# Kernel tuning notes

Measured on AMD Instinct MI355X. Metric: run time of the kernel, lower is better.

The kernel has to match this reference:

```python
import jax, jax.numpy as jnp
import numpy as np

N = 100000   # num_nodes
D = 128      # input_dim
DO = 128     # output_dim
V = 3        # num_views/relations
E = 500000   # edges per view
C = 2        # num_classes
H = D // 2   # label-attention hidden
VH = DO // 2 # view-attention hidden
EPS = 1e-5


def setup_inputs() -> dict:
    key = jax.random.key(0)
    ks = jax.random.split(key, 20)
    s = 0.05
    def nrm(k, shape):
        return jax.random.normal(k, shape, dtype=jnp.float32) * s
    return {
        'features': jax.random.normal(ks[0], (N, D), dtype=jnp.float32),
        'edge_src': jax.random.randint(ks[1], (V, E), 0, N, dtype=jnp.int32),
        'edge_dst': jax.random.randint(ks[2], (V, E), 0, N, dtype=jnp.int32),
        'edge_w': jax.random.uniform(ks[3], (V, E), dtype=jnp.float32),
        'clsW': nrm(ks[4], (D, C)), 'clsb': jnp.zeros((C,), jnp.float32),
        'attW1': nrm(ks[5], (C, D, H)), 'attb1': jnp.zeros((C, H), jnp.float32),
        'attW2': nrm(ks[6], (C, H)), 'attb2': jnp.zeros((C,), jnp.float32),
        'att_bias': jnp.float32(0.1),
        'relW': nrm(ks[7], (V, D, DO)), 'relb': jnp.zeros((V, DO), jnp.float32),
        'gateW': nrm(ks[8], (V, DO, DO)), 'gateb': jnp.zeros((V, DO), jnp.float32),
        'view_pref': jax.random.normal(ks[9], (V, DO), dtype=jnp.float32),
        'vattW1': nrm(ks[10], (DO, VH)), 'vattb1': jnp.zeros((VH,), jnp.float32),
        'vattW2': nrm(ks[11], (VH,)), 'vattb2': jnp.float32(0.0),
        'selfW': nrm(ks[12], (D, DO)), 'selfb': jnp.zeros((DO,), jnp.float32),
        'featW': nrm(ks[13], (D, DO)), 'featb': jnp.zeros((DO,), jnp.float32),
        'fusW': nrm(ks[14], (2 * DO, DO)), 'fusb': jnp.zeros((DO,), jnp.float32),
        'ln_g': jnp.ones((DO,), jnp.float32), 'ln_b': jnp.zeros((DO,), jnp.float32),
    }


def reference(features, edge_src, edge_dst, edge_w,
              clsW, clsb, attW1, attb1, attW2, attb2, att_bias,
              relW, relb, gateW, gateb,
              view_pref, vattW1, vattb1, vattW2, vattb2,
              selfW, selfb, featW, featb, fusW, fusb, ln_g, ln_b):
    # --- LabelAwareAttention ---
    class_probs = jax.nn.softmax(features @ clsW + clsb, axis=-1)          # [N,C]
    h = jax.nn.relu(jnp.einsum('nd,cdh->cnh', features, attW1) + attb1[:, None, :])
    scores = jax.nn.sigmoid(jnp.einsum('cnh,ch->cn', h, attW2) + attb2[:, None])
    node_att = jnp.sum(scores.T * class_probs, axis=-1) + att_bias         # [N]

    # --- per-view RelationAggregator (num_relations=1 -> relation weight is 1) ---
    src_f = features[edge_src]                                             # [V,E,D]
    msg = (jnp.einsum('ved,vdo->veo', src_f, relW) + relb[:, None, :]) \
          * edge_w[..., None]                                              # [V,E,DO]
    agg = jax.vmap(lambda m, d: jax.ops.segment_sum(m, d, num_segments=N))(
        msg, edge_dst)                                                     # [V,N,DO]
    gate = jax.nn.sigmoid(jnp.einsum('vno,vop->vnp', agg, gateW) + gateb[:, None, :])
    view_out = gate * agg                                                  # [V,N,DO]

    # --- ViewLevelAttention ---
    vh = jax.nn.relu(jnp.einsum('vno,oh->vnh', view_out * view_pref[:, None, :], vattW1) + vattb1)
    vscores = jnp.einsum('vnh,h->vn', vh, vattW2) + vattb2                 # [V,N]
    vweights = jax.nn.softmax(vscores, axis=0)                             # softmax over views
    combined = jnp.sum(view_out * vweights[..., None], axis=0)             # [N,DO]

    # --- fusion + residual + layer norm (dropout=0, eval) ---
    self_out = features @ selfW + selfb
    transformed = features @ featW + featb
    weighted = combined * node_att[:, None]
    fused = jax.nn.relu(jnp.concatenate([self_out, weighted], axis=-1) @ fusW + fusb)
    out = fused + transformed
    mu = jnp.mean(out, axis=-1, keepdims=True)
    var = jnp.var(out, axis=-1, keepdims=True)
    out = (out - mu) / jnp.sqrt(var + EPS) * ln_g + ln_b
    return out, class_probs
```

## Files before the change

kernel.cpp:

```cpp
#include <hip/hip_runtime.h>
#include <hip/hip_bf16.h>

#define NN 100000
#define DD 128
#define VV 3
#define EE 500000
#define TOT (VV * NN)
#define NB ((TOT + 255) / 256)
#define RGB ((NN + 127) / 128)

typedef unsigned short u16;
typedef unsigned int u32;
typedef short s8v __attribute__((ext_vector_type(8)));
typedef float f4v __attribute__((ext_vector_type(4)));

__device__ __forceinline__ float bf2f(u16 u) {
    return __uint_as_float(((u32)u) << 16);
}
__device__ __forceinline__ u16 f2bf(float f) {
    u32 x = __float_as_uint(f);
    u32 r = (x + 0x7fffu + ((x >> 16) & 1u)) >> 16;
    return (u16)r;
}

// ... 64 lines not shown
        int flat = rep * NT + tid;
        int kk = flat >> 5;
        int c4 = flat & 31;
        float4 q = *reinterpret_cast<const float4*>(src + kk * 128 + c4 * 4);
        *reinterpret_cast<float4*>(Ws + kk * WSTR + c4 * 4) = q;
    }
}

template<int XSTR, int NT>
__device__ __forceinline__ void stage_x_f32(float* Xs, const float* __restrict__ src, int tid) {
    #pragma unroll
    for (int rep = 0; rep < 1024 / NT; ++rep) {
        int flat = rep * NT + tid;
        int n = flat >> 5;
        int c4 = flat & 31;
        float4 q = *reinterpret_cast<const float4*>(src + (size_t)n * 128 + c4 * 4);
        *reinterpret_cast<float4*>(Xs + n * XSTR + c4 * 4) = q;
    }
}

template<int XSTR, int NT>
__device__ __forceinline__ void stage_x_bf16(float* Xs, const u16* __restrict__ src, int tid) {
    #pragma unroll
    for (int rep = 0; rep < 512 / NT; ++rep) {
        int flat = rep * NT + tid;
        int n = flat >> 4;
        int c8 = flat & 15;
        uint4 q = *reinterpret_cast<const uint4*>(src + (size_t)n * 128 + c8 * 8);
        float* d = Xs + n * XSTR + c8 * 8;
        d[0] = bf2f((u16)(q.x & 0xffffu)); d[1] = bf2f((u16)(q.x >> 16));
        d[2] = bf2f((u16)(q.y & 0xffffu)); d[3] = bf2f((u16)(q.y >> 16));
        d[4] = bf2f((u16)(q.z & 0xffffu)); d[5] = bf2f((u16)(q.z >> 16));
        d[6] = bf2f((u16)(q.w & 0xffffu)); d[7] = bf2f((u16)(q.w >> 16));
    }
}

__global__ void prep_kernel(const float* __restrict__ selfW, const float* __restrict__ selfb,
                            const float* __restrict__ fusW, const float* __restrict__ fusb,
                            float* __restrict__ Wsf, float* __restrict__ c1) {
    int o = threadIdx.x;
    int k = blockIdx.x;
    if (k < 128) {
        float acc = 0.f;
        for (int m = 0; m < 128; ++m)
            acc += selfW[k * 128 + m] * fusW[m * 128 + o];
        Wsf[k * 128 + o] = acc;
    } else {
        float acc = 0.f;
        for (int m = 0; m < 128; ++m)
            acc += selfb[m] * fusW[m * 128 + o];
        c1[o] = acc + fusb[o];
    }
}

__global__ __launch_bounds__(128) void wprep_kernel(
        const float* __restrict__ relW, const float* __restrict__ gateW,
        u16* __restrict__ relWb, u16* __restrict__ gateWb) {
    int k = threadIdx.x;
    int n = blockIdx.x & 127;
    int v = blockIdx.x >> 7;
    size_t o = ((size_t)v * 128 + n) * 128 + k;
    size_t i = ((size_t)v * 128 + k) * 128 + n;
    relWb[o]  = f2bf(relW[i]);
    gateWb[o] = f2bf(gateW[i]);
}

// ... 180 lines not shown
        u16* __restrict__ aggB, float* __restrict__ wsum) {
    long long t = (long long)blockIdx.x * 256 + threadIdx.x;
    int lane = (int)(t & 31);
    int eg = (int)(t >> 5);
    int v = eg / EE;
    int src = 0, dst = 0; float w = 0.f;
    if (lane == 0) {
        src = esrc[eg]; dst = edst[eg]; w = ew[eg];
    }
    src = __shfl(src, 0, 32);
    dst = __shfl(dst, 0, 32);
    w   = __shfl(w, 0, 32);
    const float* fr = feat + (size_t)src * DD + lane * 4;
    float4 q = *reinterpret_cast<const float4*>(fr);
    u16* outp = aggB + ((size_t)v * NN + dst) * DD + lane * 4;
    atomAddBf16x2(outp,     w * q.x, w * q.y);
    atomAddBf16x2(outp + 2, w * q.z, w * q.w);
    if (lane == 0) atomicAdd(wsum + v * NN + dst, w);
}

__global__ __launch_bounds__(256) void label_mfma_kernel(
        const u16* __restrict__ featB, const u16* __restrict__ attW1B,
        const float* __restrict__ clsW, const float* __restrict__ clsb,
        const float* __restrict__ attb1, const float* __restrict__ attW2,
        const float* __restrict__ attb2, const float* __restrict__ att_bias,
        float* __restrict__ node_att, float* __restrict__ probs_out) {
    __shared__ u16 Xs[128][136];
    __shared__ u16 Wt[128][72];
    int tid = threadIdx.x;
    int wv = tid >> 6, lane = tid & 63;
    int quad = lane >> 4, l15 = lane & 15;
    int row0 = blockIdx.x * 128;

    #pragma unroll
    for (int rep = 0; rep < 8; ++rep) {
        int flat = rep * 256 + tid;
        int n = flat >> 4, c8 = flat & 15;
        int gr = row0 + n; if (gr >= NN) gr = NN - 1;
        uint4 q = *reinterpret_cast<const uint4*>(featB + (size_t)gr * DD + c8 * 8);
        *reinterpret_cast<uint4*>(&Xs[n][c8 * 8]) = q;
    }

    f4v acc[2][8];
    #pragma unroll
    for (int rt = 0; rt < 2; ++rt)
        #pragma unroll
        for (int c = 0; c < 8; ++c)
            acc[rt][c] = f4v{0.f, 0.f, 0.f, 0.f};

    #pragma unroll
    for (int h = 0; h < 2; ++h) {
        #pragma unroll
        for (int rep = 0; rep < 4; ++rep) {
            int flat = rep * 256 + tid;
            int n = flat >> 3, c8 = flat & 7;
            uint4 q = *reinterpret_cast<const uint4*>(attW1B + (size_t)n * DD + h * 64 + c8 * 8);
            *reinterpret_cast<uint4*>(&Wt[n][c8 * 8]) = q;
        }
        __syncthreads();
        #pragma unroll
        for (int t = 0; t < 2; ++t) {
            int kl = t * 32 + quad * 8;
            s8v a0 = *reinterpret_cast<const s8v*>(&Xs[wv * 32 + l15][h * 64 + kl]);
            s8v a1 = *reinterpret_cast<const s8v*>(&Xs[wv * 32 + 16 + l15][h * 64 + kl]);
            #pragma unroll
            for (int c = 0; c < 8; ++c) {
                s8v b = *reinterpret_cast<const s8v*>(&Wt[c * 16 + l15][kl]);
                acc[0][c] = __builtin_amdgcn_mfma_f32_16x16x32_bf16(a0, b, acc[0][c], 0, 0, 0);
                acc[1][c] = __builtin_amdgcn_mfma_f32_16x16x32_bf16(a1, b, acc[1][c], 0, 0, 0);
            }
        }
        __syncthreads();
    }

    float ab1[8], aw2[8];
    #pragma unroll
    for (int c = 0; c < 8; ++c) {
        int col = c * 16 + l15;
        ab1[c] = attb1[col];
        aw2[c] = attW2[col];
    }
    float cw0[8], cw1[8];
    #pragma unroll
    for (int j = 0; j < 8; ++j) {
        int k = l15 * 8 + j;
        cw0[j] = clsW[k * 2];
        cw1[j] = clsW[k * 2 + 1];
    }
    float cb0 = clsb[0], cb1 = clsb[1];
    float b20 = attb2[0], b21 = attb2[1];
    float abias = att_bias[0];

    #pragma unroll
    for (int rt = 0; rt < 2; ++rt)
        #pragma unroll
        for (int r = 0; r < 4; ++r) {
            int n = wv * 32 + rt * 16 + quad * 4 + r;
            int gr = row0 + n;
            float p0 = 0.f, p1 = 0.f;
            #pragma unroll
            for (int c = 0; c < 4; ++c) {
                float hv = acc[rt][c][r] + ab1[c];
                hv = hv > 0.f ? hv : 0.f;
                p0 += hv * aw2[c];
            }
            #pragma unroll
// ... 93 lines not shown
    __syncthreads();
    if (tid < 64) {
        int n = tid >> 1, cc = tid & 1;
        float l = 0.f;
        for (int k = 0; k < 128; k += 4) {
            float4 x = *reinterpret_cast<const float4*>(&Xs[n][k]);
            l += x.x * clsW[(k + 0) * 2 + cc];
            l += x.y * clsW[(k + 1) * 2 + cc];
            l += x.z * clsW[(k + 2) * 2 + cc];
            l += x.w * clsW[(k + 3) * 2 + cc];
        }
        Lsc[n * 2 + cc] = l + clsb[cc];
        float s = 0.f;
        for (int u = 0; u < 16; ++u) s += red[n * 33 + cc * 16 + u];
        s += attb2[cc];
        Ssc[n * 2 + cc] = 1.f / (1.f + expf(-s));
    }
    __syncthreads();
    if (tid < 32) {
        int n = tid;
        float l0 = Lsc[n * 2], l1 = Lsc[n * 2 + 1];
        float m = fmaxf(l0, l1);
        float e0 = expf(l0 - m), e1 = expf(l1 - m);
        float inv = 1.f / (e0 + e1);
        float p0 = e0 * inv, p1 = e1 * inv;
        float na = p0 * Ssc[n * 2] + p1 * Ssc[n * 2 + 1] + att_bias[0];
        int row = row0 + n;
        node_att[row] = na;
        probs_out[row * 2]     = p0;
        probs_out[row * 2 + 1] = p1;
    }
}

__global__ __launch_bounds__(256, 3) void relgate_mfma_kernel(
        const u16* __restrict__ relWb, const float* __restrict__ relb,
        const u16* __restrict__ W12b, const float* __restrict__ rgb,
        const float* __restrict__ gateb,
        const u16* __restrict__ vattW1p, const float* __restrict__ vattb1,
        const float* __restrict__ vattW2, const float* __restrict__ vattb2,
        u16* __restrict__ aggB, const float* __restrict__ wsum,
        float* __restrict__ vscores) {
    __shared__ u16 Wf[128][136];
    __shared__ u16 Wt[128][72];
    int tid = threadIdx.x;
    int wv = tid >> 6, lane = tid & 63;
    int quad = lane >> 4, l15 = lane & 15;
    int v = blockIdx.y;
    int row0 = blockIdx.x * 128;
    const size_t vbase = (size_t)v * NN;

    #pragma unroll
    for (int rep = 0; rep < 8; ++rep) {
        int flat = rep * 256 + tid;
        int n = flat >> 4, c8 = flat & 15;
        int gr = row0 + n; if (gr >= NN) gr = NN - 1;
        uint4 q = *reinterpret_cast<const uint4*>(aggB + (vbase + gr) * DD + c8 * 8);
        *reinterpret_cast<uint4*>(&Wf[n][c8 * 8]) = q;
    }
    __syncthreads();

    s8v af[2][2][2];
    #pragma unroll
    for (int h = 0; h < 2; ++h)
        #pragma unroll
        for (int t = 0; t < 2; ++t) {
            int kl = h * 64 + t * 32 + quad * 8;
            af[h][t][0] = *reinterpret_cast<const s8v*>(&Wf[wv * 32 + l15][kl]);
            af[h][t][1] = *reinterpret_cast<const s8v*>(&Wf[wv * 32 + 16 + l15][kl]);
        }
    __syncthreads();

    const u16* W1 = relWb + (size_t)v * DD * DD;
    const u16* W2 = W12b + (size_t)v * DD * DD;
    #pragma unroll
    for (int rep = 0; rep < 8; ++rep) {
        int flat = rep * 256 + tid;
        int n = flat >> 4, c8 = flat & 15;
        *reinterpret_cast<uint4*>(&Wf[n][c8 * 8]) =
            *reinterpret_cast<const uint4*>(W1 + (size_t)n * DD + c8 * 8);
    }
    #pragma unroll
    for (int rep = 0; rep < 4; ++rep) {
        int flat = rep * 256 + tid;
        int n = flat >> 3, c8 = flat & 7;
        *reinterpret_cast<uint4*>(&Wt[n][c8 * 8]) =
            *reinterpret_cast<const uint4*>(W2 + (size_t)n * DD + c8 * 8);
    }
    __syncthreads();

    f4v acc1[2][8], acc2[2][8];
    #pragma unroll
    for (int rt = 0; rt < 2; ++rt)
        #pragma unroll
        for (int c = 0; c < 8; ++c) {
            acc1[rt][c] = f4v{0.f, 0.f, 0.f, 0.f};
            acc2[rt][c] = f4v{0.f, 0.f, 0.f, 0.f};
        }

    #pragma unroll
    for (int h = 0; h < 2; ++h)
        #pragma unroll
        for (int t = 0; t < 2; ++t) {
            int kl = h * 64 + t * 32 + quad * 8;
            #pragma unroll
            for (int c = 0; c < 8; ++c) {
                s8v b = *reinterpret_cast<const s8v*>(&Wf[c * 16 + l15][kl]);
                acc1[0][c] = __builtin_amdgcn_mfma_f32_16x16x32_bf16(af[h][t][0], b, acc1[0][c], 0, 0, 0);
                acc1[1][c] = __builtin_amdgcn_mfma_f32_16x16x32_bf16(af[h][t][1], b, acc1[1][c], 0, 0, 0);
            }
        }
    #pragma unroll
    for (int t = 0; t < 2; ++t) {
        int kl = t * 32 + quad * 8;
        #pragma unroll
        for (int c = 0; c < 8; ++c) {
            s8v b = *reinterpret_cast<const s8v*>(&Wt[c * 16 + l15][kl]);
            acc2[0][c] = __builtin_amdgcn_mfma_f32_16x16x32_bf16(af[0][t][0], b, acc2[0][c], 0, 0, 0);
            acc2[1][c] = __builtin_amdgcn_mfma_f32_16x16x32_bf16(af[0][t][1], b, acc2[1][c], 0, 0, 0);
        }
    }
    __syncthreads();

    #pragma unroll
    for (int rep = 0; rep < 4; ++rep) {
        int flat = rep * 256 + tid;
        int n = flat >> 3, c8 = flat & 7;
        *reinterpret_cast<uint4*>(&Wt[n][c8 * 8]) =
            *reinterpret_cast<const uint4*>(W2 + (size_t)n * DD + 64 + c8 * 8);
    }
    __syncthreads();
    #pragma unroll
    for (int t = 0; t < 2; ++t) {
        int kl = t * 32 + quad * 8;
        #pragma unroll
        for (int c = 0; c < 8; ++c) {
            s8v b = *reinterpret_cast<const s8v*>(&Wt[c * 16 + l15][kl]);
            acc2[0][c] = __builtin_amdgcn_mfma_f32_16x16x32_bf16(af[1][t][0], b, acc2[0][c], 0, 0, 0);
            acc2[1][c] = __builtin_amdgcn_mfma_f32_16x16x32_bf16(af[1][t][1], b, acc2[1][c], 0, 0, 0);
        }
    }

    float wsn[2][4];
    #pragma unroll
    for (int rt = 0; rt < 2; ++rt)
        #pragma unroll
        for (int r = 0; r < 4; ++r) {
            int gr = row0 + wv * 32 + rt * 16 + quad * 4 + r;
            wsn[rt][r] = wsum[vbase + (gr < NN ? gr : NN - 1)];
        }
    float rb[8], rg2[8], gb[8];
    #pragma unroll
    for (int c = 0; c < 8; ++c) {
        int col = c * 16 + l15;
        rb[c]  = relb[v * DD + col];
        rg2[c] = rgb[v * DD + col];
        gb[c]  = gateb[v * DD + col];
    }
    #pragma unroll
    for (int rt = 0; rt < 2; ++rt)
        #pragma unroll
        for (int c = 0; c < 8; ++c)
            #pragma unroll
            for (int r = 0; r < 4; ++r) {
                float a = acc1[rt][c][r] + wsn[rt][r] * rb[c];
                float g = fsigmoid(acc2[rt][c][r] + wsn[rt][r] * rg2[c] + gb[c]);
                Wf[wv * 32 + rt * 16 + quad * 4 + r][c * 16 + l15] = f2bf(g * a);
            }
    __syncthreads();

    {
        const u16* Wv = vattW1p + (size_t)v * 64 * DD;
        #pragma unroll
        for (int rep = 0; rep < 4; ++rep) {
            int flat = rep * 256 + tid;
            int n = flat >> 4, c8 = flat & 15;
            uint4 q = *reinterpret_cast<const uint4*>(Wv + (size_t)n * DD + c8 * 8);
            int half = c8 >> 3;
            *reinterpret_cast<uint4*>(&Wt[half * 64 + n][(c8 & 7) * 8]) = q;
        }
    }
    s8v a2[2][2][2];
    #pragma unroll
    for (int h = 0; h < 2; ++h)
        #pragma unroll
        for (int t = 0; t < 2; ++t) {
            int kl = h * 64 + t * 32 + quad * 8;
            a2[h][t][0] = *reinterpret_cast<const s8v*>(&Wf[wv * 32 + l15][kl]);
            a2[h][t][1] = *reinterpret_cast<const s8v*>(&Wf[wv * 32 + 16 + l15][kl]);
        }
    #pragma unroll
    for (int rep = 0; rep < 8; ++rep) {
        int flat = rep * 256 + tid;
        int n = flat >> 4, c8 = flat & 15;
        int gr = row0 + n;
        if (gr < NN)
            *reinterpret_cast<uint4*>(aggB + (vbase + gr) * DD + c8 * 8) =
                *reinterpret_cast<const uint4*>(&Wf[n][c8 * 8]);
    }
    __syncthreads();

    f4v acc3[2][4];
    #pragma unroll
    for (int rt = 0; rt < 2; ++rt)
        #pragma unroll
        for (int c = 0; c < 4; ++c)
            acc3[rt][c] = f4v{0.f, 0.f, 0.f, 0.f};
    #pragma unroll
    for (int h = 0; h < 2; ++h)
        #pragma unroll
        for (int t = 0; t < 2; ++t) {
            int kl = t * 32 + quad * 8;
            #pragma unroll
            for (int c = 0; c < 4; ++c) {
                s8v b = *reinterpret_cast<const s8v*>(&Wt[h * 64 + c * 16 + l15][kl]);
                acc3[0][c] = __builtin_amdgcn_mfma_f32_16x16x32_bf16(a2[h][t][0], b, acc3[0][c], 0, 0, 0);
                acc3[1][c] = __builtin_amdgcn_mfma_f32_16x16x32_bf16(a2[h][t][1], b, acc3[1][c], 0, 0, 0);
            }
        }
    float vb1[4], vw2[4];
    #pragma unroll
    for (int c = 0; c < 4; ++c) {
        int col = c * 16 + l15;
        vb1[c] = vattb1[col];
        vw2[c] = vattW2[col];
    }
    float vb2 = vattb2[0];
    #pragma unroll
    for (int rt = 0; rt < 2; ++rt)
        #pragma unroll
        for (int r = 0; r < 4; ++r) {
            float p = 0.f;
            #pragma unroll
            for (int c = 0; c < 4; ++c) {
                float hv = acc3[rt][c][r] + vb1[c];
                hv = hv > 0.f ? hv : 0.f;
                p += hv * vw2[c];
            }
            #pragma unroll
            for (int m = 1; m < 16; m <<= 1)
                p += __shfl_xor(p, m);
            int gr = row0 + wv * 32 + rt * 16 + quad * 4 + r;
            if (l15 == 0 && gr < NN)
                vscores[vbase + gr] = p + vb2;
        }
}

__global__ __launch_bounds__(256) void relgate_kernel(
        const float* __restrict__ relW, const float* __restrict__ relb,
        const float* __restrict__ gateW, const float* __restrict__ gateb,
        u16* __restrict__ aggB, const float* __restrict__ wsum) {
    __shared__ float Xs[32][128];
    __shared__ float Ws[64][132];
    int tid = threadIdx.x;
    int v = blockIdx.y;
    int row0 = blockIdx.x * 32;
    u16* base = aggB + ((size_t)v * NN + row0) * DD;
    stage_x_bf16<128, 256>(&Xs[0][0], base, tid);
    int to = tid & 31, tn = tid >> 5;
    int o0 = to * 4, n0 = tn * 4;
    float acc[4][4] = {};
    const float* W1 = relW + (size_t)v * DD * DD;
    for (int half = 0; half < 2; ++half) {
        __syncthreads();
        stage_w_f32<132, 256>(&Ws[0][0], W1 + half * 64 * DD, tid);
        __syncthreads();
        gemm16<128, 132>(acc, &Xs[0][0], &Ws[0][0], n0, o0, half * 64);
    }
    float wsn[4], rb[4];
    #pragma unroll
    for (int i = 0; i < 4; ++i) wsn[i] = wsum[v * NN + row0 + n0 + i];
    #pragma unroll
    for (int j = 0; j < 4; ++j) rb[j] = relb[v * DD + o0 + j];
    #pragma unroll
    for (int i = 0; i < 4; ++i)
        #pragma unroll
        for (int j = 0; j < 4; ++j) acc[i][j] += wsn[i] * rb[j];
    __syncthreads();
// ... 159 lines not shown
        #pragma unroll
        for (int t = 0; t < 2; ++t) {
            int kl = h * 64 + t * 32 + quad * 8;
            af[h][t][0] = *reinterpret_cast<const s8v*>(&Wf[wv * 32 + l15][kl]);
            af[h][t][1] = *reinterpret_cast<const s8v*>(&Wf[wv * 32 + 16 + l15][kl]);
        }
    __syncthreads();

    #pragma unroll
    for (int rep = 0; rep < 8; ++rep) {
        int flat = rep * 256 + tid;
        int n = flat >> 4, c8 = flat & 15;
        *reinterpret_cast<uint4*>(&Wf[n][c8 * 8]) =
            *reinterpret_cast<const uint4*>(WsfB + (size_t)n * DD + c8 * 8);
    }
    #pragma unroll
    for (int rep = 0; rep < 4; ++rep) {
        int flat = rep * 256 + tid;
        int n = flat >> 3, c8 = flat & 7;
        *reinterpret_cast<uint4*>(&Wt[n][c8 * 8]) =
            *reinterpret_cast<const uint4*>(featWB + (size_t)n * DD + c8 * 8);
    }
    __syncthreads();

    f4v acc1[2][8], acc2[2][8];
    #pragma unroll
    for (int rt = 0; rt < 2; ++rt)
        #pragma unroll
        for (int c = 0; c < 8; ++c) {
            acc1[rt][c] = f4v{0.f, 0.f, 0.f, 0.f};
            acc2[rt][c] = f4v{0.f, 0.f, 0.f, 0.f};
        }

    #pragma unroll
    for (int h = 0; h < 2; ++h)
        #pragma unroll
        for (int t = 0; t < 2; ++t) {
            int kl = h * 64 + t * 32 + quad * 8;
            #pragma unroll
            for (int c = 0; c < 8; ++c) {
                s8v b = *reinterpret_cast<const s8v*>(&Wf[c * 16 + l15][kl]);
                acc1[0][c] = __builtin_amdgcn_mfma_f32_16x16x32_bf16(af[h][t][0], b, acc1[0][c], 0, 0, 0);
                acc1[1][c] = __builtin_amdgcn_mfma_f32_16x16x32_bf16(af[h][t][1], b, acc1[1][c], 0, 0, 0);
            }
        }
    #pragma unroll
    for (int t = 0; t < 2; ++t) {
        int kl = t * 32 + quad * 8;
        #pragma unroll
        for (int c = 0; c < 8; ++c) {
            s8v b = *reinterpret_cast<const s8v*>(&Wt[c * 16 + l15][kl]);
            acc2[0][c] = __builtin_amdgcn_mfma_f32_16x16x32_bf16(af[0][t][0], b, acc2[0][c], 0, 0, 0);
            acc2[1][c] = __builtin_amdgcn_mfma_f32_16x16x32_bf16(af[0][t][1], b, acc2[1][c], 0, 0, 0);
        }
    }
    __syncthreads();
    #pragma unroll
    for (int rep = 0; rep < 4; ++rep) {
        int flat = rep * 256 + tid;
        int n = flat >> 3, c8 = flat & 7;
        *reinterpret_cast<uint4*>(&Wt[n][c8 * 8]) =
            *reinterpret_cast<const uint4*>(featWB + (size_t)n * DD + 64 + c8 * 8);
    }
    __syncthreads();
    #pragma unroll
    for (int t = 0; t < 2; ++t) {
        int kl = t * 32 + quad * 8;
        #pragma unroll
        for (int c = 0; c < 8; ++c) {
            s8v b = *reinterpret_cast<const s8v*>(&Wt[c * 16 + l15][kl]);
            acc2[0][c] = __builtin_amdgcn_mfma_f32_16x16x32_bf16(af[1][t][0], b, acc2[0][c], 0, 0, 0);
            acc2[1][c] = __builtin_amdgcn_mfma_f32_16x16x32_bf16(af[1][t][1], b, acc2[1][c], 0, 0, 0);
        }
    }

    #pragma unroll
    for (int rep = 0; rep < 8; ++rep) {
        int flat = rep * 256 + tid;
        int n = flat >> 4, c8 = flat & 15;
        int gr = row0 + n; if (gr >= NN) gr = NN - 1;
        size_t off = (size_t)gr * DD + c8 * 8;
        uint4 q0 = *reinterpret_cast<const uint4*>(aggB + off);
        uint4 q1 = *reinterpret_cast<const uint4*>(aggB + (size_t)NN * DD + off);
        uint4 q2 = *reinterpret_cast<const uint4*>(aggB + 2 * (size_t)NN * DD + off);
        const float* rwp = reinterpret_cast<const float*>(&Wf[n][128]);
        float w0 = rwp[0], w1 = rwp[1], w2 = rwp[2];
        u32 o[4];
        const u32* a = &q0.x; const u32* b = &q1.x; const u32* c = &q2.x;
        #pragma unroll
        for (int j = 0; j < 4; ++j) {
            float lo = bf2f((u16)(a[j] & 0xffffu)) * w0 + bf2f((u16)(b[j] & 0xffffu)) * w1
                     + bf2f((u16)(c[j] & 0xffffu)) * w2;
            float hi = bf2f((u16)(a[j] >> 16)) * w0 + bf2f((u16)(b[j] >> 16)) * w1
                     + bf2f((u16)(c[j] >> 16)) * w2;
            o[j] = (u32)f2bf(lo) | ((u32)f2bf(hi) << 16);
        }
        uint4 r; r.x = o[0]; r.y = o[1]; r.z = o[2]; r.w = o[3];
        *reinterpret_cast<uint4*>(&Wf[n][c8 * 8]) = r;
    }
    __syncthreads();

    #pragma unroll
    for (int rep = 0; rep < 4; ++rep) {
        int flat = rep * 256 + tid;
        int n = flat >> 3, c8 = flat & 7;
        *reinterpret_cast<uint4*>(&Wt[n][c8 * 8]) =
            *reinterpret_cast<const uint4*>(fusWbB + (size_t)n * DD + c8 * 8);
// ... 210 lines not shown
    u16* WsfB   = gateWb + (size_t)VV * DD * DD;
    u16* featWB = WsfB + DD * DD;
    u16* fusWbB = featWB + DD * DD;
    u16* attW1B = fusWbB + DD * DD;
    u16* vattW1p = attW1B + DD * DD;
    u16* W12b   = vattW1p + (size_t)VV * 64 * DD;
    float* rgb  = (float*)(W12b + (size_t)VV * DD * DD);
    int*   C    = (int*)(rgb + VV * DD);
    int*   bs   = C + (size_t)TOT;
    int2*  bsw  = (int2*)(bs + NB + 1);
    u16* featB  = (u16*)(bsw + (size_t)VV * EE);
    size_t needed = (size_t)((char*)(featB + (size_t)NN * DD) - (char*)d_ws);

    float* outp  = (float*)d_out;
    float* probs = outp + (size_t)NN * DD;

    prep_kernel<<<129, 128, 0, stream>>>(selfW, selfb, fusW, fusb, Wsf, c1);
    if (ws_size >= needed) {
        featconv_kernel<<<12500, 256, 0, stream>>>(feat, featB);
        wprep_kernel<<<384, 128, 0, stream>>>(relW, gateW, relWb, gateWb);
        wprep2_kernel<<<128, 128, 0, stream>>>(Wsf, featW, fusW, WsfB, featWB, fusWbB);
        wprep3_kernel<<<128, 128, 0, stream>>>(attW1, attW1B);
        wprep4_kernel<<<192, 128, 0, stream>>>(vattW1, view_pref, vattW1p);
        wprep5_kernel<<<VV * 129, 128, 0, stream>>>(relW, gateW, relb, W12b, rgb);
        label_mfma_kernel<<<RGB, 256, 0, stream>>>(featB, attW1B, clsW, clsb, attb1,
                                                   attW2, attb2, att_bias, natt, probs);
        hipMemsetAsync(C, 0, (size_t)TOT * sizeof(int), stream);
        count_kernel<<<(VV * EE + 255) / 256, 256, 0, stream>>>(edst, C);
        scanA_kernel<<<NB, 256, 0, stream>>>(C, bs);
        scanB_kernel<<<1, 1024, 0, stream>>>(bs);
        scanC_kernel<<<NB, 256, 0, stream>>>(C, bs);
        fill_kernel<<<(VV * EE + 255) / 256, 256, 0, stream>>>(esrc, edst, ew, C, bsw);
        gather_kernel<<<(VV * NN) / 4, 256, 0, stream>>>(featB, C, bsw, aggB, wsum);
        relgate_mfma_kernel<<<dim3(RGB, 3), 256, 0, stream>>>(relWb, relb, W12b, rgb, gateb,
                                                              vattW1p, vattb1, vattW2, vattb2,
                                                              aggB, wsum, vsc);
        final_mfma_kernel<<<RGB, 256, 0, stream>>>(featB, aggB, vsc, natt,
                                                   WsfB, featWB, fusWbB,
                                                   c1, featb, ln_g, ln_b, outp);
    } else {
        label_kernel<<<3125, 256, 0, stream>>>(feat, clsW, clsb, attW1, attb1, attW2, attb2,
                                               att_bias, natt, probs);
        hipMemsetAsync(d_ws, 0,
                       (size_t)VV * NN * DD * sizeof(u16) + (size_t)VV * NN * sizeof(float),
                       stream);
        scatter_kernel<<<187500, 256, 0, stream>>>(esrc, edst, ew, feat, aggB, wsum);
        relgate_kernel<<<dim3(3125, 3), 256, 0, stream>>>(relW, relb, gateW, gateb, aggB, wsum);
        vatt_kernel<<<dim3(3125, 3), 128, 0, stream>>>(aggB, view_pref, vattW1, vattb1,
                                                       vattW2, vattb2, vsc);
        combine_kernel<<<12500, 256, 0, stream>>>(aggB, vsc, natt);
        final_kernel<<<3125, 256, 0, stream>>>(feat, aggB, Wsf, c1, fusW, featW, featb,
                                               ln_g, ln_b, outp);
    }
}
```

Measured before the change: 661.3 us.

## Loop views inside relgate kernel, shrink shared memory, load A fragments from global

The relgate MFMA kernel now handles all three views in one block with an in-kernel loop instead of a 3-wide grid. It drops the separate Wt buffer by staging the rel and gate weight halves side by side in one shared tile. A fragments now load straight from global memory, vatt weights are read from global, and launch bounds are raised to 4 blocks per CU to gain occupancy. In exchange the grid shrinks to about 782 blocks, the views run serially inside each block, and extra barriers plus uncoalesced fragment loads are added. Label and final kernels are refactored onto shared helper functions, and label now stages the first weight half together with X under one barrier.

```diff
diff --git a/kernel.cpp b/kernel.cpp
--- a/kernel.cpp
+++ b/kernel.cpp
@@ -120,6 +120,128 @@
         d[2] = bf2f((u16)(q.y & 0xffffu)); d[3] = bf2f((u16)(q.y >> 16));
         d[4] = bf2f((u16)(q.z & 0xffffu)); d[5] = bf2f((u16)(q.z >> 16));
         d[6] = bf2f((u16)(q.w & 0xffffu)); d[7] = bf2f((u16)(q.w >> 16));
+    }
+}
+
+
+__device__ __forceinline__ void stageWf(u16 (*Wf)[136], const u16* __restrict__ src, int tid) {
+    #pragma unroll
+    for (int rep = 0; rep < 8; ++rep) {
+        int flat = rep * 256 + tid;
+        int n = flat >> 4, c8 = flat & 15;
+        *reinterpret_cast<uint4*>(&Wf[n][c8 * 8]) =
+            *reinterpret_cast<const uint4*>(src + (size_t)n * DD + c8 * 8);
+    }
+}
+
+__device__ __forceinline__ void stageWtHalf(u16 (*Wt)[72], const u16* __restrict__ src, int tid) {
+    #pragma unroll
+    for (int rep = 0; rep < 4; ++rep) {
+        int flat = rep * 256 + tid;
+        int n = flat >> 3, c8 = flat & 7;
+        *reinterpret_cast<uint4*>(&Wt[n][c8 * 8]) =
+            *reinterpret_cast<const uint4*>(src + (size_t)n * DD + c8 * 8);
+    }
+}
+
+__device__ __forceinline__ void stageHalf2(u16 (*Wf)[136], const u16* __restrict__ A,
+                                           const u16* __restrict__ B, int tid) {
+    #pragma unroll
+    for (int rep = 0; rep < 4; ++rep) {
+        int flat = rep * 256 + tid;
+        int n = flat >> 3, c8 = flat & 7;
+        *reinterpret_cast<uint4*>(&Wf[n][c8 * 8]) =
+            *reinterpret_cast<const uint4*>(A + (size_t)n * DD + c8 * 8);
+        *reinterpret_cast<uint4*>(&Wf[n][64 + c8 * 8]) =
+            *reinterpret_cast<const uint4*>(B + (size_t)n * DD + c8 * 8);
+    }
+}
+
+__device__ __forceinline__ void stageX(u16 (*Wf)[136], const u16* __restrict__ src,
+                                       int row0, int tid) {
+    #pragma unroll
+    for (int rep = 0; rep < 8; ++rep) {
+        int flat = rep * 256 + tid;
+        int n = flat >> 4, c8 = flat & 15;
+        int gr = row0 + n; if (gr >= NN) gr = NN - 1;
+        *reinterpret_cast<uint4*>(&Wf[n][c8 * 8]) =
+            *reinterpret_cast<const uint4*>(src + (size_t)gr * DD + c8 * 8);
+    }
+}
+
+__device__ __forceinline__ void loadFrags(s8v af[2][2][2], u16 (*Wf)[136],
+                                          int wv, int l15, int quad) {
+    #pragma unroll
+    for (int h = 0; h < 2; ++h)
+        #pragma unroll
+        for (int t = 0; t < 2; ++t) {
+            int kl = h * 64 + t * 32 + quad * 8;
+            af[h][t][0] = *reinterpret_cast<const s8v*>(&Wf[wv * 32 + l15][kl]);
+            af[h][t][1] = *reinterpret_cast<const s8v*>(&Wf[wv * 32 + 16 + l15][kl]);
+        }
+}
+
+__device__ __forceinline__ void loadFragsG(s8v af[2][2][2], const u16* __restrict__ X,
+                                           int row0, int wv, int l15, int quad) {
+    int r0 = row0 + wv * 32 + l15;
+    int r1 = r0 + 16;
+    if (r0 >= NN) r0 = NN - 1;
+    if (r1 >= NN) r1 = NN - 1;
+    #pragma unroll
+    for (int h = 0; h < 2; ++h)
+        #pragma unroll
+        for (int t = 0; t < 2; ++t) {
+            int kl = h * 64 + t * 32 + quad * 8;
+            af[h][t][0] = *reinterpret_cast<const s8v*>(X + (size_t)r0 * DD + kl);
+            af[h][t][1] = *reinterpret_cast<const s8v*>(X + (size_t)r1 * DD + kl);
+        }
+}
+
+__device__ __forceinline__ void mfmaWt8(f4v acc[2][8], const s8v af[2][2][2], int h,
+                                        u16 (*Wt)[72], int l15, int quad) {
+    #pragma unroll
+    for (int t = 0; t < 2; ++t) {
+        int kl = t * 32 + quad * 8;
+        #pragma unroll
+        for (int c = 0; c < 8; ++c) {
+            s8v b = *reinterpret_cast<const s8v*>(&Wt[c * 16 + l15][kl]);
+            acc[0][c] = __builtin_amdgcn_mfma_f32_16x16x32_bf16(af[h][t][0], b, acc[0][c], 0, 0, 0);
+            acc[1][c] = __builtin_amdgcn_mfma_f32_16x16x32_bf16(af[h][t][1], b, acc[1][c], 0, 0, 0);
+        }
+    }
+}
+
+__device__ __forceinline__ void mfmaWfFull(f4v acc[2][8], const s8v af[2][2][2],
+                                           u16 (*Wf)[136], int l15, int quad) {
+    #pragma unroll
+    for (int h = 0; h < 2; ++h)
+        #pragma unroll
+        for (int t = 0; t < 2; ++t) {
+            int kl = h * 64 + t * 32 + quad * 8;
+            #pragma unroll
+            for (int c = 0; c < 8; ++c) {
+                s8v b = *reinterpret_cast<const s8v*>(&Wf[c * 16 + l15][kl]);
+                acc[0][c] = __builtin_amdgcn_mfma_f32_16x16x32_bf16(af[h][t][0], b, acc[0][c], 0, 0, 0);
+                acc[1][c] = __builtin_amdgcn_mfma_f32_16x16x32_bf16(af[h][t][1], b, acc[1][c], 0, 0, 0);
+            }
+        }
+}
+
+__device__ __forceinline__ void mfmaHalf2(f4v acc1[2][8], f4v acc2[2][8],
+                                          const s8v af[2][2][2], int h,
+                                          u16 (*Wf)[136], int l15, int quad) {
+    #pragma unroll
+    for (int t = 0; t < 2; ++t) {
+        int kl = t * 32 + quad * 8;
+        #pragma unroll
+        for (int c = 0; c < 8; ++c) {
+            s8v bA = *reinterpret_cast<const s8v*>(&Wf[c * 16 + l15][kl]);
+            s8v bB = *reinterpret_cast<const s8v*>(&Wf[c * 16 + l15][64 + kl]);
+            acc1[0][c] = __builtin_amdgcn_mfma_f32_16x16x32_bf16(af[h][t][0], bA, acc1[0][c], 0, 0, 0);
+            acc1[1][c] = __builtin_amdgcn_mfma_f32_16x16x32_bf16(af[h][t][1], bA, acc1[1][c], 0, 0, 0);
+            acc2[0][c] = __builtin_amdgcn_mfma_f32_16x16x32_bf16(af[h][t][0], bB, acc2[0][c], 0, 0, 0);
+            acc2[1][c] = __builtin_amdgcn_mfma_f32_16x16x32_bf16(af[h][t][1], bB, acc2[1][c], 0, 0, 0);
+        }
     }
 }
 
@@ -366,46 +488,22 @@
     int quad = lane >> 4, l15 = lane & 15;
     int row0 = blockIdx.x * 128;
 
-    #pragma unroll
-    for (int rep = 0; rep < 8; ++rep) {
-        int flat = rep * 256 + tid;
-        int n = flat >> 4, c8 = flat & 15;
-        int gr = row0 + n; if (gr >= NN) gr = NN - 1;
-        uint4 q = *reinterpret_cast<const uint4*>(featB + (size_t)gr * DD + c8 * 8);
-        *reinterpret_cast<uint4*>(&Xs[n][c8 * 8]) = q;
-    }
-
+    stageX(Xs, featB, row0, tid);
+    stageWtHalf(Wt, attW1B, tid);
+    __syncthreads();
+    s8v af[2][2][2];
+    loadFrags(af, Xs, wv, l15, quad);
     f4v acc[2][8];
     #pragma unroll
     for (int rt = 0; rt < 2; ++rt)
         #pragma unroll
         for (int c = 0; c < 8; ++c)
             acc[rt][c] = f4v{0.f, 0.f, 0.f, 0.f};
-
-    #pragma unroll
-    for (int h = 0; h < 2; ++h) {
-        #pragma unroll
-        for (int rep = 0; rep < 4; ++rep) {
-            int flat = rep * 256 + tid;
-            int n = flat >> 3, c8 = flat & 7;
-            uint4 q = *reinterpret_cast<const uint4*>(attW1B + (size_t)n * DD + h * 64 + c8 * 8);
-            *reinterpret_cast<uint4*>(&Wt[n][c8 * 8]) = q;
-        }
-        __syncthreads();
-        #pragma unroll
-        for (int t = 0; t < 2; ++t) {
-            int kl = t * 32 + quad * 8;
-            s8v a0 = *reinterpret_cast<const s8v*>(&Xs[wv * 32 + l15][h * 64 + kl]);
-            s8v a1 = *reinterpret_cast<const s8v*>(&Xs[wv * 32 + 16 + l15][h * 64 + kl]);
-            #pragma unroll
-            for (int c = 0; c < 8; ++c) {
-                s8v b = *reinterpret_cast<const s8v*>(&Wt[c * 16 + l15][kl]);
-                acc[0][c] = __builtin_amdgcn_mfma_f32_16x16x32_bf16(a0, b, acc[0][c], 0, 0, 0);
-                acc[1][c] = __builtin_amdgcn_mfma_f32_16x16x32_bf16(a1, b, acc[1][c], 0, 0, 0);
-            }
-        }
-        __syncthreads();
-    }
+    mfmaWt8(acc, af, 0, Wt, l15, quad);
+    __syncthreads();
+    stageWtHalf(Wt, attW1B + 64, tid);
+    __syncthreads();
+    mfmaWt8(acc, af, 1, Wt, l15, quad);
 
     float ab1[8], aw2[8];
     #pragma unroll
@@ -565,217 +663,145 @@
     }
 }
 
-__global__ __launch_bounds__(256, 3) void relgate_mfma_kernel(
+__global__ __launch_bounds__(256, 4) void relgate_mfma_kernel(
         const u16* __restrict__ relWb, const float* __restrict__ relb,
-        const u16* __restrict__ W12b, const float* __restrict__ rgb,
+        const u16* __restrict__ W12b, const float* __restrict__ rgbv,
         const float* __restrict__ gateb,
         const u16* __restrict__ vattW1p, const float* __restrict__ vattb1,
         const float* __restrict__ vattW2, const float* __restrict__ vattb2,
         u16* __restrict__ aggB, const float* __restrict__ wsum,
         float* __restrict__ vscores) {
     __shared__ u16 Wf[128][136];
-    __shared__ u16 Wt[128][72];
     int tid = threadIdx.x;
     int wv = tid >> 6, lane = tid & 63;
     int quad = lane >> 4, l15 = lane & 15;
-    int v = blockIdx.y;
     int row0 = blockIdx.x * 128;
-    const size_t vbase = (size_t)v * NN;
-
-    #pragma unroll
-    for (int rep = 0; rep < 8; ++rep) {
-        int flat = rep * 256 + tid;
-        int n = flat >> 4, c8 = flat & 15;
-        int gr = row0 + n; if (gr >= NN) gr = NN - 1;
-        uint4 q = *reinterpret_cast<const uint4*>(aggB + (vbase + gr) * DD + c8 * 8);
-        *reinterpret_cast<uint4*>(&Wf[n][c8 * 8]) = q;
-    }
-    __syncthreads();
-
-    s8v af[2][2][2];
-    #pragma unroll
-    for (int h = 0; h < 2; ++h)
-        #pragma unroll
-        for (int t = 0; t < 2; ++t) {
-            int kl = h * 64 + t * 32 + quad * 8;
-            af[h][t][0] = *reinterpret_cast<const s8v*>(&Wf[wv * 32 + l15][kl]);
-            af[h][t][1] = *reinterpret_cast<const s8v*>(&Wf[wv * 32 + 16 + l15][kl]);
-        }
-    __syncthreads();
-
-    const u16* W1 = relWb + (size_t)v * DD * DD;
-    const u16* W2 = W12b + (size_t)v * DD * DD;
-    #pragma unroll
-    for (int rep = 0; rep < 8; ++rep) {
-        int flat = rep * 256 + tid;
-        int n = flat >> 4, c8 = flat & 15;
-        *reinterpret_cast<uint4*>(&Wf[n][c8 * 8]) =
-            *reinterpret_cast<const uint4*>(W1 + (size_t)n * DD + c8 * 8);
-    }
-    #pragma unroll
-    for (int rep = 0; rep < 4; ++rep) {
-        int flat = rep * 256 + tid;
-        int n = flat >> 3, c8 = flat & 7;
-        *reinterpret_cast<uint4*>(&Wt[n][c8 * 8]) =
-            *reinterpret_cast<const uint4*>(W2 + (size_t)n * DD + c8 * 8);
-    }
-    __syncthreads();
-
-    f4v acc1[2][8], acc2[2][8];
-    #pragma unroll
-    for (int rt = 0; rt < 2; ++rt)
+
+    for (int v = 0; v < VV; ++v) {
+        const size_t vbase = (size_t)v * NN;
+
+        s8v af[2][2][2];
+        loadFragsG(af, aggB + vbase * DD, row0, wv, l15, quad);
+
+        const u16* W1 = relWb + (size_t)v * DD * DD;
+        const u16* W2 = W12b + (size_t)v * DD * DD;
+
+        float wsn[2][4];
+        #pragma unroll
+        for (int rt = 0; rt < 2; ++rt)
+            #pragma unroll
+            for (int r = 0; r < 4; ++r) {
+                int gr = row0 + wv * 32 + rt * 16 + quad * 4 + r;
+                wsn[rt][r] = wsum[vbase + (gr < NN ? gr : NN - 1)];
+            }
+
+        f4v acc1[2][8], acc2[2][8];
+        #pragma unroll
+        for (int rt = 0; rt < 2; ++rt)
+            #pragma unroll
+            for (int c = 0; c < 8; ++c) {
+                acc1[rt][c] = f4v{0.f, 0.f, 0.f, 0.f};
+                acc2[rt][c] = f4v{0.f, 0.f, 0.f, 0.f};
+            }
+
+        __syncthreads();
+        stageHalf2(Wf, W1, W2, tid);
+        __syncthreads();
+        mfmaHalf2(acc1, acc2, af, 0, Wf, l15, quad);
+        __syncthreads();
+        stageHalf2(Wf, W1 + 64, W2 + 64, tid);
+        __syncthreads();
+        mfmaHalf2(acc1, acc2, af, 1, Wf, l15, quad);
+
+        u32 gpk[2][8][2];
         #pragma unroll
         for (int c = 0; c < 8; ++c) {
-            acc1[rt][c] = f4v{0.f, 0.f, 0.f, 0.f};
-            acc2[rt][c] = f4v{0.f, 0.f, 0.f, 0.f};
-        }
-
-    #pragma unroll
-    for (int h = 0; h < 2; ++h)
-        #pragma unroll
-        for (int t = 0; t < 2; ++t) {
-            int kl = h * 64 + t * 32 + quad * 8;
-            #pragma unroll
-            for (int c = 0; c < 8; ++c) {
-                s8v b = *reinterpret_cast<const s8v*>(&Wf[c * 16 + l15][kl]);
-                acc1[0][c] = __builtin_amdgcn_mfma_f32_16x16x32_bf16(af[h][t][0], b, acc1[0][c], 0, 0, 0);
-                acc1[1][c] = __builtin_amdgcn_mfma_f32_16x16x32_bf16(af[h][t][1], b, acc1[1][c], 0, 0, 0);
+            int col = c * 16 + l15;
+            float rg2 = rgbv[v * DD + col];
+            float gb2 = gateb[v * DD + col];
+            #pragma unroll
+            for (int rt = 0; rt < 2; ++rt)
+                #pragma unroll
+                for (int rp = 0; rp < 2; ++rp) {
+                    float g0 = fsigmoid(acc2[rt][c][2 * rp]     + wsn[rt][2 * rp] * rg2 + gb2);
+                    float g1 = fsigmoid(acc2[rt][c][2 * rp + 1] + wsn[rt][2 * rp + 1] * rg2 + gb2);
+                    gpk[rt][c][rp] = (u32)f2bf(g0) | ((u32)f2bf(g1) << 16);
+                }
+        }
+        __syncthreads();
+
+        #pragma unroll
+        for (int c = 0; c < 8; ++c) {
+            float rbc = relb[v * DD + c * 16 + l15];
+            #pragma unroll
+            for (int rt = 0; rt < 2; ++rt)
+                #pragma unroll
+                for (int r = 0; r < 4; ++r) {
+                    float a = acc1[rt][c][r] + wsn[rt][r] * rbc;
+                    u32 gp = gpk[rt][c][r >> 1];
+                    float g = bf2f((u16)((r & 1) ? (gp >> 16) : (gp & 0xffffu)));
+                    Wf[wv * 32 + rt * 16 + quad * 4 + r][c * 16 + l15] = f2bf(g * a);
+                }
+        }
+
+        #pragma unroll
+        for (int rep = 0; rep < 8; ++rep) {
+            int n = wv * 32 + rep * 4 + quad;
+            int gr = row0 + n;
+            if (gr < NN)
+                *reinterpret_cast<uint4*>(aggB + (vbase + gr) * DD + l15 * 8) =
+                    *reinterpret_cast<const uint4*>(&Wf[n][l15 * 8]);
+        }
+
+        s8v a2[2][2][2];
+        loadFrags(a2, Wf, wv, l15, quad);
+        const u16* Wv = vattW1p + (size_t)v * 64 * DD;
+        f4v acc3[2][4];
+        #pragma unroll
+        for (int rt = 0; rt < 2; ++rt)
+            #pragma unroll
+            for (int c = 0; c < 4; ++c)
+                acc3[rt][c] = f4v{0.f, 0.f, 0.f, 0.f};
+        #pragma unroll
+        for (int h = 0; h < 2; ++h)
+            #pragma unroll
+            for (int t = 0; t < 2; ++t) {
+                int kl = t * 32 + quad * 8;
+                #pragma unroll
+                for (int c = 0; c < 4; ++c) {
+                    s8v b = *reinterpret_cast<const s8v*>(
+                        Wv + (size_t)(c * 16 + l15) * DD + h * 64 + kl);
+                    acc3[0][c] = __builtin_amdgcn_mfma_f32_16x16x32_bf16(a2[h][t][0], b, acc3[0][c], 0, 0, 0);
+                    acc3[1][c] = __builtin_amdgcn_mfma_f32_16x16x32_bf16(a2[h][t][1], b, acc3[1][c], 0, 0, 0);
+                }
             }
-        }
-    #pragma unroll
-    for (int t = 0; t < 2; ++t) {
-        int kl = t * 32 + quad * 8;
-        #pragma unroll
-        for (int c = 0; c < 8; ++c) {
-            s8v b = *reinterpret_cast<const s8v*>(&Wt[c * 16 + l15][kl]);
-            acc2[0][c] = __builtin_amdgcn_mfma_f32_16x16x32_bf16(af[0][t][0], b, acc2[0][c], 0, 0, 0);
-            acc2[1][c] = __builtin_amdgcn_mfma_f32_16x16x32_bf16(af[0][t][1], b, acc2[1][c], 0, 0, 0);
-        }
-    }
-    __syncthreads();
-
-    #pragma unroll
-    for (int rep = 0; rep < 4; ++rep) {
-        int flat = rep * 256 + tid;
-        int n = flat >> 3, c8 = flat & 7;
-        *reinterpret_cast<uint4*>(&Wt[n][c8 * 8]) =
-            *reinterpret_cast<const uint4*>(W2 + (size_t)n * DD + 64 + c8 * 8);
-    }
-    __syncthreads();
-    #pragma unroll
-    for (int t = 0; t < 2; ++t) {
-        int kl = t * 32 + quad * 8;
-        #pragma unroll
-        for (int c = 0; c < 8; ++c) {
-            s8v b = *reinterpret_cast<const s8v*>(&Wt[c * 16 + l15][kl]);
-            acc2[0][c] = __builtin_amdgcn_mfma_f32_16x16x32_bf16(af[1][t][0], b, acc2[0][c], 0, 0, 0);
-            acc2[1][c] = __builtin_amdgcn_mfma_f32_16x16x32_bf16(af[1][t][1], b, acc2[1][c], 0, 0, 0);
-        }
-    }
-
-    float wsn[2][4];
-    #pragma unroll
-    for (int rt = 0; rt < 2; ++rt)
-        #pragma unroll
-        for (int r = 0; r < 4; ++r) {
-            int gr = row0 + wv * 32 + rt * 16 + quad * 4 + r;
-            wsn[rt][r] = wsum[vbase + (gr < NN ? gr : NN - 1)];
-        }
-    float rb[8], rg2[8], gb[8];
-    #pragma unroll
-    for (int c = 0; c < 8; ++c) {
-        int col = c * 16 + l15;
-        rb[c]  = relb[v * DD + col];
-        rg2[c] = rgb[v * DD + col];
-        gb[c]  = gateb[v * DD + col];
-    }
-    #pragma unroll
-    for (int rt = 0; rt < 2; ++rt)
-        #pragma unroll
-        for (int c = 0; c < 8; ++c)
+        float vb1[4], vw2[4];
+        #pragma unroll
+        for (int c = 0; c < 4; ++c) {
+            int col = c * 16 + l15;
+            vb1[c] = vattb1[col];
+            vw2[c] = vattW2[col];
+        }
+        float vb2 = vattb2[0];
+        #pragma unroll
+        for (int rt = 0; rt < 2; ++rt)
             #pragma unroll
             for (int r = 0; r < 4; ++r) {
-                float a = acc1[rt][c][r] + wsn[rt][r] * rb[c];
-                float g = fsigmoid(acc2[rt][c][r] + wsn[rt][r] * rg2[c] + gb[c]);
-                Wf[wv * 32 + rt * 16 + quad * 4 + r][c * 16 + l15] = f2bf(g * a);
+                float p = 0.f;
+                #pragma unroll
+                for (int c = 0; c < 4; ++c) {
+                    float hv = acc3[rt][c][r] + vb1[c];
+                    hv = hv > 0.f ? hv : 0.f;
+                    p += hv * vw2[c];
+                }
+                #pragma unroll
+                for (int m = 1; m < 16; m <<= 1)
+                    p += __shfl_xor(p, m);
+                int gr = row0 + wv * 32 + rt * 16 + quad * 4 + r;
+                if (l15 == 0 && gr < NN)
+                    vscores[vbase + gr] = p + vb2;
             }
-    __syncthreads();
-
-    {
-        const u16* Wv = vattW1p + (size_t)v * 64 * DD;
-        #pragma unroll
-        for (int rep = 0; rep < 4; ++rep) {
-            int flat = rep * 256 + tid;
-            int n = flat >> 4, c8 = flat & 15;
-            uint4 q = *reinterpret_cast<const uint4*>(Wv + (size_t)n * DD + c8 * 8);
-            int half = c8 >> 3;
-            *reinterpret_cast<uint4*>(&Wt[half * 64 + n][(c8 & 7) * 8]) = q;
-        }
-    }
-    s8v a2[2][2][2];
-    #pragma unroll
-    for (int h = 0; h < 2; ++h)
-        #pragma unroll
-        for (int t = 0; t < 2; ++t) {
-            int kl = h * 64 + t * 32 + quad * 8;
-            a2[h][t][0] = *reinterpret_cast<const s8v*>(&Wf[wv * 32 + l15][kl]);
-            a2[h][t][1] = *reinterpret_cast<const s8v*>(&Wf[wv * 32 + 16 + l15][kl]);
-        }
-    #pragma unroll
-    for (int rep = 0; rep < 8; ++rep) {
-        int flat = rep * 256 + tid;
-        int n = flat >> 4, c8 = flat & 15;
-        int gr = row0 + n;
-        if (gr < NN)
-            *reinterpret_cast<uint4*>(aggB + (vbase + gr) * DD + c8 * 8) =
-                *reinterpret_cast<const uint4*>(&Wf[n][c8 * 8]);
-    }
-    __syncthreads();
-
-    f4v acc3[2][4];
-    #pragma unroll
-    for (int rt = 0; rt < 2; ++rt)
-        #pragma unroll
-        for (int c = 0; c < 4; ++c)
-            acc3[rt][c] = f4v{0.f, 0.f, 0.f, 0.f};
-    #pragma unroll
-    for (int h = 0; h < 2; ++h)
-        #pragma unroll
-        for (int t = 0; t < 2; ++t) {
-            int kl = t * 32 + quad * 8;
-            #pragma unroll
-            for (int c = 0; c < 4; ++c) {
-                s8v b = *reinterpret_cast<const s8v*>(&Wt[h * 64 + c * 16 + l15][kl]);
-                acc3[0][c] = __builtin_amdgcn_mfma_f32_16x16x32_bf16(a2[h][t][0], b, acc3[0][c], 0, 0, 0);
-                acc3[1][c] = __builtin_amdgcn_mfma_f32_16x16x32_bf16(a2[h][t][1], b, acc3[1][c], 0, 0, 0);
-            }
-        }
-    float vb1[4], vw2[4];
-    #pragma unroll
-    for (int c = 0; c < 4; ++c) {
-        int col = c * 16 + l15;
-        vb1[c] = vattb1[col];
-        vw2[c] = vattW2[col];
-    }
-    float vb2 = vattb2[0];
-    #pragma unroll
-    for (int rt = 0; rt < 2; ++rt)
-        #pragma unroll
-        for (int r = 0; r < 4; ++r) {
-            float p = 0.f;
-            #pragma unroll
-            for (int c = 0; c < 4; ++c) {
-                float hv = acc3[rt][c][r] + vb1[c];
-                hv = hv > 0.f ? hv : 0.f;
-                p += hv * vw2[c];
-            }
-            #pragma unroll
-            for (int m = 1; m < 16; m <<= 1)
-                p += __shfl_xor(p, m);
-            int gr = row0 + wv * 32 + rt * 16 + quad * 4 + r;
-            if (l15 == 0 && gr < NN)
-                vscores[vbase + gr] = p + vb2;
-        }
+    }
 }
 
 __global__ __launch_bounds__(256) void relgate_kernel(
@@ -1001,28 +1027,8 @@
             acc2[rt][c] = f4v{0.f, 0.f, 0.f, 0.f};
         }
 
-    #pragma unroll
-    for (int h = 0; h < 2; ++h)
-        #pragma unroll
-        for (int t = 0; t < 2; ++t) {
-            int kl = h * 64 + t * 32 + quad * 8;
-            #pragma unroll
-            for (int c = 0; c < 8; ++c) {
-                s8v b = *reinterpret_cast<const s8v*>(&Wf[c * 16 + l15][kl]);
-                acc1[0][c] = __builtin_amdgcn_mfma_f32_16x16x32_bf16(af[h][t][0], b, acc1[0][c], 0, 0, 0);
-                acc1[1][c] = __builtin_amdgcn_mfma_f32_16x16x32_bf16(af[h][t][1], b, acc1[1][c], 0, 0, 0);
-            }
-        }
-    #pragma unroll
-    for (int t = 0; t < 2; ++t) {
-        int kl = t * 32 + quad * 8;
-        #pragma unroll
-        for (int c = 0; c < 8; ++c) {
-            s8v b = *reinterpret_cast<const s8v*>(&Wt[c * 16 + l15][kl]);
-            acc2[0][c] = __builtin_amdgcn_mfma_f32_16x16x32_bf16(af[0][t][0], b, acc2[0][c], 0, 0, 0);
-            acc2[1][c] = __builtin_amdgcn_mfma_f32_16x16x32_bf16(af[0][t][1], b, acc2[1][c], 0, 0, 0);
-        }
-    }
+    mfmaWfFull(acc1, af, Wf, l15, quad);
+    mfmaWt8(acc2, af, 0, Wt, l15, quad);
     __syncthreads();
     #pragma unroll
     for (int rep = 0; rep < 4; ++rep) {
@@ -1032,16 +1038,7 @@
             *reinterpret_cast<const uint4*>(featWB + (size_t)n * DD + 64 + c8 * 8);
     }
     __syncthreads();
-    #pragma unroll
-    for (int t = 0; t < 2; ++t) {
-        int kl = t * 32 + quad * 8;
-        #pragma unroll
-        for (int c = 0; c < 8; ++c) {
-            s8v b = *reinterpret_cast<const s8v*>(&Wt[c * 16 + l15][kl]);
-            acc2[0][c] = __builtin_amdgcn_mfma_f32_16x16x32_bf16(af[1][t][0], b, acc2[0][c], 0, 0, 0);
-            acc2[1][c] = __builtin_amdgcn_mfma_f32_16x16x32_bf16(af[1][t][1], b, acc2[1][c], 0, 0, 0);
-        }
-    }
+    mfmaWt8(acc2, af, 1, Wt, l15, quad);
 
     #pragma unroll
     for (int rep = 0; rep < 8; ++rep) {
@@ -1318,9 +1315,9 @@
         scanC_kernel<<<NB, 256, 0, stream>>>(C, bs);
         fill_kernel<<<(VV * EE + 255) / 256, 256, 0, stream>>>(esrc, edst, ew, C, bsw);
         gather_kernel<<<(VV * NN) / 4, 256, 0, stream>>>(featB, C, bsw, aggB, wsum);
-        relgate_mfma_kernel<<<dim3(RGB, 3), 256, 0, stream>>>(relWb, relb, W12b, rgb, gateb,
-                                                              vattW1p, vattb1, vattW2, vattb2,
-                                                              aggB, wsum, vsc);
+        relgate_mfma_kernel<<<RGB, 256, 0, stream>>>(relWb, relb, W12b, rgb, gateb,
+                                                     vattW1p, vattb1, vattW2, vattb2,
+                                                     aggB, wsum, vsc);
         final_mfma_kernel<<<RGB, 256, 0, stream>>>(featB, aggB, vsc, natt,
                                                    WsfB, featWB, fusWbB,
                                                    c1, featb, ln_g, ln_b, outp);
```

After: 942.3 us. +42.5%, slower.
